# Kernel tuning notes

Hardware: AMD Instinct MI355X
Metric: run time of the kernel (lower is better)

The kernel has to match this reference:

```python
import jax, jax.numpy as jnp
import numpy as np

# ---- grid / frustum config (from default grid_config & data_config) ----
DB = (1.0, 60.0, 1.0)                 # dbound
OGH, OGW, DS = 256, 704, 16           # input size, downsample
FH, FW = OGH // DS, OGW // DS         # 16, 44
DEPTH = int(round((DB[1] - DB[0]) / DB[2]))  # 59 depth bins
NX0, NX1, NZ = 128, 128, 1            # BEV grid
DX = np.array([0.8, 0.8, 20.0], np.float32)
BX = np.array([-51.2 + 0.4, -51.2 + 0.4, 0.0], np.float32)  # row0 + dx/2


def _frustum():
    # (D, FH, FW, 3): pixel (u, v, depth)
    ds = jnp.broadcast_to(jnp.arange(DB[0], DB[1], DB[2], dtype=jnp.float32).reshape(-1, 1, 1), (DEPTH, FH, FW))
    xs = jnp.broadcast_to(jnp.linspace(0.0, OGW - 1.0, FW, dtype=jnp.float32).reshape(1, 1, FW), (DEPTH, FH, FW))
    ys = jnp.broadcast_to(jnp.linspace(0.0, OGH - 1.0, FH, dtype=jnp.float32).reshape(1, FH, 1), (DEPTH, FH, FW))
    return jnp.stack([xs, ys, ds], axis=-1)


def _geometry(rots, trans, intrins, post_rots, post_trans, bda):
    # pixel frustum -> ego-frame 3D points; (B, N, D, FH, FW, 3)
    pts = _frustum() - post_trans[:, :, None, None, None, :]
    pts = jnp.einsum('bnij,bndhwj->bndhwi', jnp.linalg.inv(post_rots), pts)
    pts = jnp.concatenate([pts[..., :2] * pts[..., 2:3], pts[..., 2:3]], axis=-1)
    comb = jnp.einsum('bnij,bnjk->bnik', rots, jnp.linalg.inv(intrins))
    pts = jnp.einsum('bnij,bndhwj->bndhwi', comb, pts) + trans[:, :, None, None, None, :]
    pts = jnp.einsum('bij,bndhwj->bndhwi', bda, pts)
    return pts


def _voxel_pool(geom, vol):
    # geom: (B,N,D,FH,FW,3), vol: (B,N,D,FH,FW,C) -> BEV (B, C*NZ, NX0, NX1)
    B, C = vol.shape[0], vol.shape[-1]
    gidx = jnp.floor((geom - (BX - DX / 2.0)) / DX).astype(jnp.int32)
    kept = ((gidx[..., 0] >= 0) & (gidx[..., 0] < NX0)
            & (gidx[..., 1] >= 0) & (gidx[..., 1] < NX1)
            & (gidx[..., 2] >= 0) & (gidx[..., 2] < NZ))
    bidx = jnp.broadcast_to(jnp.arange(B, dtype=jnp.int32).reshape(B, 1, 1, 1, 1), gidx.shape[:-1])
    flat = ((bidx * NZ + gidx[..., 2]) * NX0 + gidx[..., 0]) * NX1 + gidx[..., 1]
    nvox = B * NZ * NX0 * NX1
    flat = jnp.where(kept, flat, nvox).reshape(-1)      # dump bucket for culled pts
    feats = vol.reshape(-1, C)
    bev = jax.ops.segment_sum(feats, flat, num_segments=nvox + 1)[:nvox]
    bev = bev.reshape(B, NZ, NX0, NX1, C)
    bev = jnp.moveaxis(bev, -1, 2).reshape(B, NZ * C, NX0, NX1)  # z-major channel cat
    return bev


def setup_inputs() -> dict:
    key = jax.random.key(0)
    B, N, CIN, CT = 4, 6, 512, 64
    k1, k2 = jax.random.split(key, 2)
    x = jax.random.normal(k1, (B, N, CIN, FH, FW), dtype=jnp.float32)
    weight = jax.random.normal(k2, (DEPTH + CT, CIN), dtype=jnp.float32) * 0.02
    bias = jnp.zeros((DEPTH + CT,), dtype=jnp.float32)
    # cam->ego rotation (cam z forward -> ego x, cam x right -> ego -y, cam y down -> ego -z)
    Rcam = jnp.asarray(np.array([[0., 0., 1.], [-1., 0., 0.], [0., -1., 0.]], np.float32))
    rots = jnp.tile(Rcam, (B, N, 1, 1))
    trans = jnp.zeros((B, N, 3), dtype=jnp.float32)
    K = jnp.asarray(np.array([[600., 0., 352.], [0., 600., 128.], [0., 0., 1.]], np.float32))
    intrins = jnp.tile(K, (B, N, 1, 1))
    post_rots = jnp.tile(jnp.eye(3, dtype=jnp.float32), (B, N, 1, 1))
    post_trans = jnp.zeros((B, N, 3), dtype=jnp.float32)
    bda = jnp.tile(jnp.eye(3, dtype=jnp.float32), (B, 1, 1))
    return dict(x=x, rots=rots, trans=trans, intrins=intrins, post_rots=post_rots,
                post_trans=post_trans, bda=bda, weight=weight, bias=bias)


def reference(x, rots, trans, intrins, post_rots, post_trans, bda, weight, bias):
    # 1x1 depth/context head (eval mode): (B,N,Cin,H,W) -> (B,N,D+C,H,W)
    out = jnp.einsum('bnchw,oc->bnohw', x, weight) + bias[None, None, :, None, None]
    depth = jax.nn.softmax(out[:, :, :DEPTH], axis=2)      # (B,N,D,H,W)
    feat = out[:, :, DEPTH:]                               # (B,N,C,H,W)
    # depth-context outer product -> frustum volume (B,N,D,H,W,C)
    vol = jnp.einsum('bndhw,bnchw->bndhwc', depth, feat)
    geom = _geometry(rots, trans, intrins, post_rots, post_trans, bda)
    bev = _voxel_pool(geom, vol)                           # (B, C*NZ, 128, 128)
    return bev, depth
```

## Files before the change

kernel.cpp:

```cpp
#include <hip/hip_runtime.h>
#include <math.h>

#define CIN   512
#define NOUT  123
#define DEPN  59
#define CT    64
#define B_    4
#define N_    6
#define FH    16
#define FW    44
#define HW    704
#define NPIX  (B_*N_*HW)
#define NX    128
#define BEV_ELEMS (B_*CT*NX*NX)
#define DEPTH_OFF BEV_ELEMS

#define WS_WB   1920
#define WS_PS   (WS_WB + 32768)
#define WS_FS   (WS_PS + NPIX*64)
#define WS_GC   (WS_FS + NPIX*64)
#define WS_C    (WS_GC + NPIX*18)
#define WS_VOX  (WS_C + B_*FW*DEPN*64)

typedef short bf16x8 __attribute__((ext_vector_type(8)));
typedef float f32x4  __attribute__((ext_vector_type(4)));

__device__ inline unsigned short f2bf(float f) {
    unsigned u = __float_as_uint(f);
    return (unsigned short)((u + 0x7fffu + ((u >> 16) & 1u)) >> 16);
}

__device__ inline void inv3d(const double* m, double* o) {
    #pragma clang fp contract(off)
    double c00 = m[4]*m[8] - m[5]*m[7];
    double c01 = m[5]*m[6] - m[3]*m[8];
    double c02 = m[3]*m[7] - m[4]*m[6];
    double det = m[0]*c00 + m[1]*c01 + m[2]*c02;
    o[0] = c00/det; o[1] = (m[2]*m[7]-m[1]*m[8])/det; o[2] = (m[1]*m[5]-m[2]*m[4])/det;
    o[3] = c01/det; o[4] = (m[0]*m[8]-m[2]*m[6])/det; o[5] = (m[2]*m[3]-m[0]*m[5])/det;
    o[6] = c02/det; o[7] = (m[1]*m[6]-m[0]*m[7])/det; o[8] = (m[0]*m[4]-m[1]*m[3])/det;
}
__device__ inline void mm3d(const double* a, const double* b, double* o) {
    #pragma clang fp contract(off)
    for (int i = 0; i < 3; ++i)
        for (int k = 0; k < 3; ++k)
            o[i*3+k] = (a[i*3+0]*b[0*3+k] + a[i*3+1]*b[1*3+k]) + a[i*3+2]*b[2*3+k];
}

__global__ __launch_bounds__(256) void k0_prep(
        const float* __restrict__ rots,  const float* __restrict__ trans,
        const float* __restrict__ intr,  const float* __restrict__ prots,
        const float* __restrict__ ptrans,const float* __restrict__ bda,
        const float* __restrict__ W,     float* __restrict__ ws,
        float* __restrict__ dout) {
    __shared__ double sTd[24][33];
    const int tid = threadIdx.x;
    const int bid = blockIdx.x;
    int gtid = bid * 256 + tid;
    int stride = gridDim.x * 256;
    float4 z = {0.f, 0.f, 0.f, 0.f};
    for (int i = gtid; i < BEV_ELEMS / 4; i += stride)
        *(float4*)(dout + 4 * (size_t)i) = z;
    unsigned short* wb = (unsigned short*)(ws + WS_WB);
    for (int i = gtid; i < 128 * CIN; i += stride) {
        int o = i >> 9, c = i & 511;
        wb[i] = (o < NOUT) ? f2bf(W[o * CIN + c]) : (unsigned short)0;
    }
    if (bid >= 66) return;
    if (tid < B_ * N_) {
        #pragma clang fp contract(off)
        int t = tid, b = t / N_;
        double* X = sTd[t];
        double PR[9], Kd[9], Rd[9], Bd[9];
        for (int i = 0; i < 9; ++i) PR[i] = (double)prots[t * 9 + i];
        for (int i = 0; i < 9; ++i) Kd[i] = (double)intr[t * 9 + i];
        for (int i = 0; i < 9; ++i) Rd[i] = (double)rots[t * 9 + i];
        for (int i = 0; i < 9; ++i) Bd[i] = (double)bda[b * 9 + i];
        double iPR[9]; inv3d(PR, iPR);
        for (int i = 0; i < 9; ++i) X[i] = iPR[i];
        for (int i = 0; i < 3; ++i) X[9 + i] = (double)ptrans[t * 3 + i];
        double iK[9];  inv3d(Kd, iK);
        double comb[9]; mm3d(Rd, iK, comb);
        for (int i = 0; i < 9; ++i) X[12 + i] = comb[i];
        for (int i = 0; i < 3; ++i) X[21 + i] = (double)trans[t * 3 + i];
        for (int i = 0; i < 9; ++i) X[24 + i] = Bd[i];
    }
    __syncthreads();
    {
        #pragma clang fp contract(off)
        int i = bid * 256 + tid;
        int b = i / (FW * 96);
        int rem = i - b * (FW * 96);
        int w = rem / 96;
        int j = rem - w * 96;
        int n = j >> 4, h = j & 15;
        const double* T = sTd[b * N_ + n];
        const double xs = (w == 43) ? 703.0 : (double)w * (703.0 / 43.0);
        const double ys = (double)(h * 17);
        const double u0 = xs - T[9];
        const double u1 = ys - T[10];
        double pA[3], pB[3];
        #pragma unroll
        for (int k = 0; k < 3; ++k) {
            pA[k] = (T[3*k]*u0 + T[3*k+1]*u1) - T[3*k+2]*T[11];
            pB[k] = T[3*k+2];
        }
        double q0c[3] = { pA[0]*pA[2], pA[0]*pB[2] + pB[0]*pA[2], pB[0]*pB[2] };
        double q1c[3] = { pA[1]*pA[2], pA[1]*pB[2] + pB[1]*pA[2], pB[1]*pB[2] };
        double q2c[3] = { pA[2], pB[2], 0.0 };
        double rc[3][3], gc[3][3];
        #pragma unroll
        for (int r = 0; r < 3; ++r)
            #pragma unroll
            for (int k = 0; k < 3; ++k)
                rc[r][k] = ((T[12+3*r]*q0c[k] + T[13+3*r]*q1c[k]) + T[14+3*r]*q2c[k])
                           + ((k == 0) ? T[21+r] : 0.0);
        #pragma unroll
        for (int g = 0; g < 3; ++g)
            #pragma unroll
            for (int k = 0; k < 3; ++k)
                gc[g][k] = (T[24+3*g]*rc[0][k] + T[25+3*g]*rc[1][k]) + T[26+3*g]*rc[2][k];
        double* dst = (double*)(ws) + WS_GC / 2 + (size_t)i * 9;
        #pragma unroll
        for (int q = 0; q < 9; ++q) dst[q] = gc[q / 3][q % 3];
    }
}

#define K1A   4608
#define K1T   13824
__global__ __launch_bounds__(256, 2) void k1_gemm(const float* __restrict__ x,
                                                  const float* __restrict__ bias,
                                                  float* __restrict__ ws,
                                                  float* __restrict__ dout) {
    __shared__ __align__(16) unsigned short s16[2 * K1T];
    const int tid = threadIdx.x;
    const int wave = tid >> 6, lane = tid & 63;
    const int l15 = lane & 15, quad = lane >> 4;
    const int bn = blockIdx.y;
    const int pixbase = blockIdx.x * 64;
    const float* xg = x + (size_t)bn * CIN * HW + pixbase;
    const unsigned short* wbg = (const unsigned short*)(ws + WS_WB);
    const int cpack = tid >> 4;
    const int pix4 = (tid & 15) * 4;
    const int wo  = tid >> 3;
    const int wsub = tid & 7;

    f32x4 acc[8] = {};
    float4 xr0, xr1, xr2, xr3;
    uint4  wr4[4];
    {
        const float* src = xg + (size_t)(4 * cpack) * HW + pix4;
        xr0 = *(const float4*)(src);
        xr1 = *(const float4*)(src + HW);
        xr2 = *(const float4*)(src + 2 * HW);
        xr3 = *(const float4*)(src + 3 * HW);
        #pragma unroll
        for (int i = 0; i < 4; ++i)
            wr4[i] = *(const uint4*)(wbg + (size_t)(wo + 32 * i) * CIN + wsub * 8);
    }
    #pragma unroll
    for (int it = 0; it < 8; ++it) {
        const int buf = it & 1;
        unsigned short* sa = s16 + buf * K1T;
        unsigned short* sb = sa + K1A;
        {
            const float* f0 = (const float*)&xr0; const float* f1 = (const float*)&xr1;
            const float* f2 = (const float*)&xr2; const float* f3 = (const float*)&xr3;
            #pragma unroll
            for (int i = 0; i < 4; ++i) {
                uint2 pk;
                pk.x = (unsigned)f2bf(f0[i]) | ((unsigned)f2bf(f1[i]) << 16);
                pk.y = (unsigned)f2bf(f2[i]) | ((unsigned)f2bf(f3[i]) << 16);
                *(uint2*)&sa[(pix4 + i) * 72 + 4 * cpack] = pk;
            }
            #pragma unroll
            for (int i = 0; i < 4; ++i)
                *(uint4*)&sb[(wo + 32 * i) * 72 + wsub * 8] = wr4[i];
        }
        if (it < 7) {
            const int ck = (it + 1) * 64;
            const float* src = xg + (size_t)(ck + 4 * cpack) * HW + pix4;
            xr0 = *(const float4*)(src);
            xr1 = *(const float4*)(src + HW);
            xr2 = *(const float4*)(src + 2 * HW);
            xr3 = *(const float4*)(src + 3 * HW);
            #pragma unroll
            for (int i = 0; i < 4; ++i)
                wr4[i] = *(const uint4*)(wbg + (size_t)(wo + 32 * i) * CIN + ck + wsub * 8);
        }
        __syncthreads();
        #pragma unroll
        for (int ks = 0; ks < 64; ks += 32) {
            const bf16x8 a = *(const bf16x8*)&sa[(wave * 16 + l15) * 72 + ks + quad * 8];
            #pragma unroll
            for (int nt = 0; nt < 8; ++nt) {
                const bf16x8 b = *(const bf16x8*)&sb[(nt * 16 + l15) * 72 + ks + quad * 8];
                acc[nt] = __builtin_amdgcn_mfma_f32_16x16x32_bf16(a, b, acc[nt], 0, 0, 0);
            }
        }
    }
    float* sred = (float*)s16;
    const int b = bn / N_, n = bn - b * N_;
    {
        float bb[8];
        #pragma unroll
        for (int nt = 0; nt < 8; ++nt) {
            int o = nt * 16 + l15;
            bb[nt] = (o < NOUT) ? bias[o] : 0.0f;
        }
        float* ps = ws + WS_PS;
        float* fs = ws + WS_FS;
        #pragma unroll
        for (int reg = 0; reg < 4; ++reg) {
            int pixl = wave * 16 + quad * 4 + reg;
            int pix = pixbase + pixl;
            int h = pix / FW, w = pix - h * FW;
            size_t row = (size_t)(b * FW + w) * 96 + n * FH + h;
            float v[4]; float m = -INFINITY;
            #pragma unroll
            for (int nt = 0; nt < 4; ++nt) {
                v[nt] = acc[nt][reg] + bb[nt];
                if (nt * 16 + l15 < DEPN) m = fmaxf(m, v[nt]);
            }
            #pragma unroll
            for (int msk = 8; msk >= 1; msk >>= 1) m = fmaxf(m, __shfl_xor(m, msk, 64));
            float e[4], s = 0.0f;
            #pragma unroll
            for (int nt = 0; nt < 4; ++nt) {
                e[nt] = (nt * 16 + l15 < DEPN) ? expf(v[nt] - m) : 0.0f;
                s += e[nt];
            }
            #pragma unroll
            for (int msk = 8; msk >= 1; msk >>= 1) s += __shfl_xor(s, msk, 64);
            const float inv = 1.0f / s;
            #pragma unroll
            for (int nt = 0; nt < 4; ++nt) {
                int o = nt * 16 + l15;
                if (o < DEPN) {
                    float p = e[nt] * inv;
                    ps[row * 64 + o] = p;
                    sred[pixl * 65 + o] = p;
                } else fs[row * 64 + (o - DEPN)] = v[nt];
            }
            #pragma unroll
            for (int nt = 4; nt < 8; ++nt) {
                int o = nt * 16 + l15;
                if (o < NOUT) fs[row * 64 + (o - DEPN)] = acc[nt][reg] + bb[nt];
            }
        }
    }
    __syncthreads();
    for (int o = wave; o < DEPN; o += 4)
        dout[DEPTH_OFF + ((size_t)bn * DEPN + o) * HW + pixbase + lane] = sred[lane * 65 + o];
}

#define DQ2 16
__global__ __launch_bounds__(256) void k2b_geom(float* __restrict__ ws,
                                                float* __restrict__ dout) {
    __shared__ float sF[96][64];
    __shared__ float sP[DQ2][100];
    __shared__ unsigned short sv16[DQ2 * 96];
    __shared__ __align__(16) double sG[96 * 9];
    __shared__ int sflag[DQ2];
    const int tid = threadIdx.x;
    const int bw = blockIdx.x;
    const int b = bw / FW;
    const int dbase = blockIdx.y * DQ2;
    const int nd = min(DQ2, DEPN - dbase);

    {
        const float* fsrc = ws + WS_FS + (size_t)bw * (96 * 64);
        const float* psrc = ws + WS_PS + (size_t)bw * (96 * 64);
        for (int i = tid; i < 96 * 16; i += 256) {
            int j = i >> 4, c4 = (i & 15) * 4;
            *(float4*)&sF[j][c4] = *(const float4*)(fsrc + j * 64 + c4);
        }
        for (int i = tid; i < 96 * 4; i += 256) {
            int j = i >> 2, q = i & 3;
            const float4 p4 = *(const float4*)(psrc + j * 64 + dbase + 4 * q);
            sP[4 * q + 0][j] = p4.x; sP[4 * q + 1][j] = p4.y;
            sP[4 * q + 2][j] = p4.z; sP[4 * q + 3][j] = p4.w;
        }
        const double2* gsrc = (const double2*)((const double*)(ws) + WS_GC / 2
                                               + (size_t)bw * (96 * 9));
        for (int i = tid; i < 432; i += 256)
            ((double2*)sG)[i] = gsrc[i];
    }
    __syncthreads();

    {
        const double BXY = (double)(-51.2000007629394531f);
        for (int idx = tid; idx < nd * 96; idx += 256) {
            int dl = idx / 96, j = idx - dl * 96;
            const double* G = &sG[j * 9];
            const double dsv = (double)(dbase + dl + 1);
            const double g0 = (G[2] * dsv + G[1]) * dsv + G[0];
            const double g1 = (G[5] * dsv + G[4]) * dsv + G[3];
            const double g2 = (G[8] * dsv + G[7]) * dsv + G[6];
            const double fx = floor((g0 - BXY) * 1.25);
            const double fy = floor((g1 - BXY) * 1.25);
            const bool keep = (fx >= 0.0) & (fx < 128.0) & (fy >= 0.0) & (fy < 128.0) &
                              (g2 >= -10.0) & (g2 < 10.0);
            sv16[idx] = keep ? (unsigned short)((int)fx * NX + (int)fy)
                             : (unsigned short)0xFFFF;
        }
    }
    __syncthreads();

    {
        const int dl = tid >> 4, s = tid & 15;
        int u = -1, mix = 0;
        const int base = dl * 96 + s * 6;
        #pragma unroll
        for (int t = 0; t < 6; ++t) {
            int v = sv16[base + t];
            if (v != 0xFFFF) { if (u < 0) u = v; else if (v != u) mix = 1; }
        }
        #pragma unroll
        for (int msk = 1; msk < 16; msk <<= 1) {
            int uo = __shfl_xor(u, msk, 64);
            int mo = __shfl_xor(mix, msk, 64);
            mix = mix | mo | ((u >= 0 && uo >= 0 && uo != u) ? 1 : 0);
            u = (u < 0) ? uo : u;
        }
        if (s == 0 && dl < nd) sflag[dl] = mix ? -2 : u;
    }
    for (int idx = tid; idx < nd * 96; idx += 256) {
        if (sv16[idx] == 0xFFFF) {
            int dl = idx / 96, j = idx - dl * 96;
            sP[dl][j] = 0.0f;
        }
    }
    __syncthreads();

    const int dl = tid >> 4, ci = tid & 15;
    if (dl < nd) {
        const int flag = sflag[dl];
        if (ci == 0)
            ((int*)(ws + WS_VOX))[bw * DEPN + dbase + dl] = (flag >= 0) ? flag : -1;
        if (flag >= 0) {
            float ax = 0.f, ay = 0.f, az = 0.f, aw = 0.f;
            for (int jj = 0; jj < 96; jj += 4) {
                const float4 pv = *(const float4*)&sP[dl][jj];
                const float4 f0 = *(const float4*)&sF[jj + 0][4 * ci];
                const float4 f1 = *(const float4*)&sF[jj + 1][4 * ci];
                const float4 f2 = *(const float4*)&sF[jj + 2][4 * ci];
                const float4 f3 = *(const float4*)&sF[jj + 3][4 * ci];
                ax = fmaf(pv.x, f0.x, ax); ay = fmaf(pv.x, f0.y, ay);
                az = fmaf(pv.x, f0.z, az); aw = fmaf(pv.x, f0.w, aw);
                ax = fmaf(pv.y, f1.x, ax); ay = fmaf(pv.y, f1.y, ay);
                az = fmaf(pv.y, f1.z, az); aw = fmaf(pv.y, f1.w, aw);
                ax = fmaf(pv.z, f2.x, ax); ay = fmaf(pv.z, f2.y, ay);
                az = fmaf(pv.z, f2.z, az); aw = fmaf(pv.z, f2.w, aw);
                ax = fmaf(pv.w, f3.x, ax); ay = fmaf(pv.w, f3.y, ay);
                az = fmaf(pv.w, f3.z, az); aw = fmaf(pv.w, f3.w, aw);
            }
            float4 st = { ax, ay, az, aw };
            *(float4*)&ws[WS_C + ((size_t)(bw * DEPN + dbase + dl)) * 64 + 4 * ci] = st;
        }
    }
    for (int d2 = 0; d2 < nd; ++d2) {
        if (sflag[d2] == -2) {
            int c = tid & 63, g = tid >> 6;
            for (int jj = 0; jj < 24; ++jj) {
                int j = g * 24 + jj;
                int v = sv16[d2 * 96 + j];
                if (v != 0xFFFF)
                    atomicAdd(dout + (((size_t)(b * CT + c)) << 14) + v,
                              sP[d2][j] * sF[j][c]);
            }
        }
    }
}

#define CHUNK 128
__global__ __launch_bounds__(256) void k2c_scatter(const float* __restrict__ ws,
                                                   float* __restrict__ dout) {
    __shared__ float acc[64][CHUNK + 4];
    __shared__ int   sVox[FW * DEPN];
    __shared__ short sMatch[FW * DEPN];
    __shared__ int   nMatch;
    const int tid = threadIdx.x;
    const int base = blockIdx.x * CHUNK;
    const int b = blockIdx.y;
    for (int i = tid; i < 64 * (CHUNK + 4); i += 256) (&acc[0][0])[i] = 0.0f;
    if (tid == 0) nMatch = 0;
    const int* vsrc = (const int*)(ws + WS_VOX) + b * (FW * DEPN);
    for (int i = tid; i < FW * DEPN; i += 256) sVox[i] = vsrc[i];
    __syncthreads();
    for (int i = tid; i < FW * DEPN; i += 256) {
        int v = sVox[i];
        if ((unsigned)(v - base) < CHUNK) {
            int m = atomicAdd(&nMatch, 1);
            sMatch[m] = (short)i;
        }
    }
    __syncthreads();
    const int c = tid & 63, quarter = tid >> 6;
    const int nm = nMatch;
    for (int m = quarter; m < nm; m += 4) {
        int e = sMatch[m];
        int lv = sVox[e] - base;
        float val = ws[WS_C + ((size_t)b * (FW * DEPN) + e) * 64 + c];
        atomicAdd(&acc[c][lv], val);
    }
    __syncthreads();
    const int wave = tid >> 6, lane = tid & 63;
    float* outb = dout + (((size_t)(b * CT)) << 14) + base;
    for (int r = wave; r < 64; r += 4) {
        float2* dst = (float2*)(outb + ((size_t)r << 14) + lane * 2);
        float2 v = *dst;
        v.x += acc[r][lane * 2];
        v.y += acc[r][lane * 2 + 1];
        *dst = v;
    }
}

extern "C" void kernel_launch(void* const* d_in, const int* in_sizes, int n_in,
                              void* d_out, int out_size, void* d_ws, size_t ws_size,
                              hipStream_t stream) {
    const float* x      = (const float*)d_in[0];
    const float* rots   = (const float*)d_in[1];
    const float* trans  = (const float*)d_in[2];
    const float* intr   = (const float*)d_in[3];
    const float* prots  = (const float*)d_in[4];
    const float* ptrans = (const float*)d_in[5];
    const float* bda    = (const float*)d_in[6];
    const float* W      = (const float*)d_in[7];
    const float* bias   = (const float*)d_in[8];
    float* out = (float*)d_out;
    float* ws  = (float*)d_ws;

    k0_prep<<<512, 256, 0, stream>>>(rots, trans, intr, prots, ptrans, bda, W, ws, out);
    k1_gemm<<<dim3(HW / 64, B_ * N_), 256, 0, stream>>>(x, bias, ws, out);
    k2b_geom<<<dim3(B_ * FW, 4), 256, 0, stream>>>(ws, out);
    k2c_scatter<<<dim3(NX * NX / CHUNK, B_), 256, 0, stream>>>(ws, out);
}
```

Baseline: 150.4 us.

## Eliminate prep kernel by fusing weight conversion, geometry, and BEV zeroing into consumers

Drops the separate k0_prep launch. The GEMM now reads fp32 weights and converts them to bf16 in-register, and it also zeroes the BEV output after its epilogue. Geometry is recomputed per block in k2b_geom into shared memory, so the double-precision geometry buffer no longer goes through global memory. A global 'mixed' flag lets the scatter kernel write its results directly instead of doing a read-modify-write when no direct atomics happened. The cost is redundant weight conversion and geometry work in every block, plus an ordering dependency: the zeroing in k1 must finish before k2b's atomics, which holds because the kernels run in stream order.

```diff
diff --git a/kernel.cpp b/kernel.cpp
--- a/kernel.cpp
+++ b/kernel.cpp
@@ -18,9 +18,9 @@
 #define WS_WB   1920
 #define WS_PS   (WS_WB + 32768)
 #define WS_FS   (WS_PS + NPIX*64)
-#define WS_GC   (WS_FS + NPIX*64)
-#define WS_C    (WS_GC + NPIX*18)
+#define WS_C    (WS_FS + NPIX*64)
 #define WS_VOX  (WS_C + B_*FW*DEPN*64)
+#define WS_MIXF (WS_VOX + B_*FW*DEPN)
 
 typedef short bf16x8 __attribute__((ext_vector_type(8)));
 typedef float f32x4  __attribute__((ext_vector_type(4)));
@@ -47,30 +47,197 @@
             o[i*3+k] = (a[i*3+0]*b[0*3+k] + a[i*3+1]*b[1*3+k]) + a[i*3+2]*b[2*3+k];
 }
 
-__global__ __launch_bounds__(256) void k0_prep(
+#define K1A   4608
+#define K1T   13824
+__global__ __launch_bounds__(256, 2) void k1_gemm(const float* __restrict__ x,
+                                                  const float* __restrict__ W,
+                                                  const float* __restrict__ bias,
+                                                  float* __restrict__ ws,
+                                                  float* __restrict__ dout) {
+    __shared__ __align__(16) unsigned short s16[2 * K1T];
+    const int tid = threadIdx.x;
+    const int wave = tid >> 6, lane = tid & 63;
+    const int l15 = lane & 15, quad = lane >> 4;
+    const int bn = blockIdx.y;
+    const int pixbase = blockIdx.x * 64;
+    const float* xg = x + (size_t)bn * CIN * HW + pixbase;
+    const int cpack = tid >> 4;
+    const int pix4 = (tid & 15) * 4;
+    const int wo  = tid >> 3;
+    const int wsub = tid & 7;
+
+    f32x4 acc[8] = {};
+    float4 xr0, xr1, xr2, xr3;
+    float4 wf[8];
+    const float4 zf4 = {0.f, 0.f, 0.f, 0.f};
+    {
+        const float* src = xg + (size_t)(4 * cpack) * HW + pix4;
+        xr0 = *(const float4*)(src);
+        xr1 = *(const float4*)(src + HW);
+        xr2 = *(const float4*)(src + 2 * HW);
+        xr3 = *(const float4*)(src + 3 * HW);
+        #pragma unroll
+        for (int i = 0; i < 4; ++i) {
+            const int o = wo + 32 * i;
+            if (o < NOUT) {
+                const float* wp = W + (size_t)o * CIN + wsub * 8;
+                wf[2 * i]     = *(const float4*)(wp);
+                wf[2 * i + 1] = *(const float4*)(wp + 4);
+            } else { wf[2 * i] = zf4; wf[2 * i + 1] = zf4; }
+        }
+    }
+    #pragma unroll
+    for (int it = 0; it < 8; ++it) {
+        const int buf = it & 1;
+        unsigned short* sa = s16 + buf * K1T;
+        unsigned short* sb = sa + K1A;
+        {
+            const float* f0 = (const float*)&xr0; const float* f1 = (const float*)&xr1;
+            const float* f2 = (const float*)&xr2; const float* f3 = (const float*)&xr3;
+            #pragma unroll
+            for (int i = 0; i < 4; ++i) {
+                uint2 pk;
+                pk.x = (unsigned)f2bf(f0[i]) | ((unsigned)f2bf(f1[i]) << 16);
+                pk.y = (unsigned)f2bf(f2[i]) | ((unsigned)f2bf(f3[i]) << 16);
+                *(uint2*)&sa[(pix4 + i) * 72 + 4 * cpack] = pk;
+            }
+            #pragma unroll
+            for (int i = 0; i < 4; ++i) {
+                const float* fw = (const float*)&wf[2 * i];
+                uint4 pk;
+                pk.x = (unsigned)f2bf(fw[0]) | ((unsigned)f2bf(fw[1]) << 16);
+                pk.y = (unsigned)f2bf(fw[2]) | ((unsigned)f2bf(fw[3]) << 16);
+                pk.z = (unsigned)f2bf(fw[4]) | ((unsigned)f2bf(fw[5]) << 16);
+                pk.w = (unsigned)f2bf(fw[6]) | ((unsigned)f2bf(fw[7]) << 16);
+                *(uint4*)&sb[(wo + 32 * i) * 72 + wsub * 8] = pk;
+            }
+        }
+        if (it < 7) {
+            const int ck = (it + 1) * 64;
+            const float* src = xg + (size_t)(ck + 4 * cpack) * HW + pix4;
+            xr0 = *(const float4*)(src);
+            xr1 = *(const float4*)(src + HW);
+            xr2 = *(const float4*)(src + 2 * HW);
+            xr3 = *(const float4*)(src + 3 * HW);
+            #pragma unroll
+            for (int i = 0; i < 4; ++i) {
+                const int o = wo + 32 * i;
+                if (o < NOUT) {
+                    const float* wp = W + (size_t)o * CIN + ck + wsub * 8;
+                    wf[2 * i]     = *(const float4*)(wp);
+                    wf[2 * i + 1] = *(const float4*)(wp + 4);
+                } else { wf[2 * i] = zf4; wf[2 * i + 1] = zf4; }
+            }
+        }
+        __syncthreads();
+        #pragma unroll
+        for (int ks = 0; ks < 64; ks += 32) {
+            const bf16x8 a = *(const bf16x8*)&sa[(wave * 16 + l15) * 72 + ks + quad * 8];
+            #pragma unroll
+            for (int nt = 0; nt < 8; ++nt) {
+                const bf16x8 b = *(const bf16x8*)&sb[(nt * 16 + l15) * 72 + ks + quad * 8];
+                acc[nt] = __builtin_amdgcn_mfma_f32_16x16x32_bf16(a, b, acc[nt], 0, 0, 0);
+            }
+        }
+    }
+    float* sred = (float*)s16;
+    const int b = bn / N_, n = bn - b * N_;
+    {
+        float bb[8];
+        #pragma unroll
+        for (int nt = 0; nt < 8; ++nt) {
+            int o = nt * 16 + l15;
+            bb[nt] = (o < NOUT) ? bias[o] : 0.0f;
+        }
+        float* ps = ws + WS_PS;
+        float* fs = ws + WS_FS;
+        #pragma unroll
+        for (int reg = 0; reg < 4; ++reg) {
+            int pixl = wave * 16 + quad * 4 + reg;
+            int pix = pixbase + pixl;
+            int h = pix / FW, w = pix - h * FW;
+            size_t row = (size_t)(b * FW + w) * 96 + n * FH + h;
+            float v[4]; float m = -INFINITY;
+            #pragma unroll
+            for (int nt = 0; nt < 4; ++nt) {
+                v[nt] = acc[nt][reg] + bb[nt];
+                if (nt * 16 + l15 < DEPN) m = fmaxf(m, v[nt]);
+            }
+            #pragma unroll
+            for (int msk = 8; msk >= 1; msk >>= 1) m = fmaxf(m, __shfl_xor(m, msk, 64));
+            float e[4], s = 0.0f;
+            #pragma unroll
+            for (int nt = 0; nt < 4; ++nt) {
+                e[nt] = (nt * 16 + l15 < DEPN) ? expf(v[nt] - m) : 0.0f;
+                s += e[nt];
+            }
+            #pragma unroll
+            for (int msk = 8; msk >= 1; msk >>= 1) s += __shfl_xor(s, msk, 64);
+            const float inv = 1.0f / s;
+            #pragma unroll
+            for (int nt = 0; nt < 4; ++nt) {
+                int o = nt * 16 + l15;
+                if (o < DEPN) {
+                    float p = e[nt] * inv;
+                    ps[row * 64 + o] = p;
+                    sred[pixl * 65 + o] = p;
+                } else fs[row * 64 + (o - DEPN)] = v[nt];
+            }
+            #pragma unroll
+            for (int nt = 4; nt < 8; ++nt) {
+                int o = nt * 16 + l15;
+                if (o < NOUT) fs[row * 64 + (o - DEPN)] = acc[nt][reg] + bb[nt];
+            }
+        }
+    }
+    __syncthreads();
+    for (int o = wave; o < DEPN; o += 4)
+        dout[DEPTH_OFF + ((size_t)bn * DEPN + o) * HW + pixbase + lane] = sred[lane * 65 + o];
+    {
+        const int gbid = bn * 11 + blockIdx.x;
+        float4 z = {0.f, 0.f, 0.f, 0.f};
+        for (int i = gbid * 256 + tid; i < BEV_ELEMS / 4; i += 264 * 256)
+            *(float4*)(dout + 4 * (size_t)i) = z;
+        if (gbid == 0 && tid == 0) ((int*)(ws + WS_MIXF))[0] = 0;
+    }
+}
+
+#define DQ2 16
+__global__ __launch_bounds__(256) void k2b_geom(
         const float* __restrict__ rots,  const float* __restrict__ trans,
         const float* __restrict__ intr,  const float* __restrict__ prots,
         const float* __restrict__ ptrans,const float* __restrict__ bda,
-        const float* __restrict__ W,     float* __restrict__ ws,
-        float* __restrict__ dout) {
-    __shared__ double sTd[24][33];
+        float* __restrict__ ws,          float* __restrict__ dout) {
+    __shared__ float sF[96][64];
+    __shared__ float sP[DQ2][100];
+    __shared__ unsigned short sv16[DQ2 * 96];
+    __shared__ __align__(16) double sG[96 * 9];
+    __shared__ double sTd[N_][33];
+    __shared__ int sflag[DQ2];
     const int tid = threadIdx.x;
-    const int bid = blockIdx.x;
-    int gtid = bid * 256 + tid;
-    int stride = gridDim.x * 256;
-    float4 z = {0.f, 0.f, 0.f, 0.f};
-    for (int i = gtid; i < BEV_ELEMS / 4; i += stride)
-        *(float4*)(dout + 4 * (size_t)i) = z;
-    unsigned short* wb = (unsigned short*)(ws + WS_WB);
-    for (int i = gtid; i < 128 * CIN; i += stride) {
-        int o = i >> 9, c = i & 511;
-        wb[i] = (o < NOUT) ? f2bf(W[o * CIN + c]) : (unsigned short)0;
-    }
-    if (bid >= 66) return;
-    if (tid < B_ * N_) {
+    const int bw = blockIdx.x;
+    const int b = bw / FW, w = bw - b * FW;
+    const int dbase = blockIdx.y * DQ2;
+    const int nd = min(DQ2, DEPN - dbase);
+
+    {
+        const float* fsrc = ws + WS_FS + (size_t)bw * (96 * 64);
+        const float* psrc = ws + WS_PS + (size_t)bw * (96 * 64);
+        for (int i = tid; i < 96 * 16; i += 256) {
+            int j = i >> 4, c4 = (i & 15) * 4;
+            *(float4*)&sF[j][c4] = *(const float4*)(fsrc + j * 64 + c4);
+        }
+        for (int i = tid; i < 96 * 4; i += 256) {
+            int j = i >> 2, q = i & 3;
+            const float4 p4 = *(const float4*)(psrc + j * 64 + dbase + 4 * q);
+            sP[4 * q + 0][j] = p4.x; sP[4 * q + 1][j] = p4.y;
+            sP[4 * q + 2][j] = p4.z; sP[4 * q + 3][j] = p4.w;
+        }
+    }
+    if (tid < N_) {
         #pragma clang fp contract(off)
-        int t = tid, b = t / N_;
-        double* X = sTd[t];
+        int t = b * N_ + tid;
+        double* X = sTd[tid];
         double PR[9], Kd[9], Rd[9], Bd[9];
         for (int i = 0; i < 9; ++i) PR[i] = (double)prots[t * 9 + i];
         for (int i = 0; i < 9; ++i) Kd[i] = (double)intr[t * 9 + i];
@@ -86,15 +253,10 @@
         for (int i = 0; i < 9; ++i) X[24 + i] = Bd[i];
     }
     __syncthreads();
-    {
+    if (tid < 96) {
         #pragma clang fp contract(off)
-        int i = bid * 256 + tid;
-        int b = i / (FW * 96);
-        int rem = i - b * (FW * 96);
-        int w = rem / 96;
-        int j = rem - w * 96;
-        int n = j >> 4, h = j & 15;
-        const double* T = sTd[b * N_ + n];
+        int j = tid, n = j >> 4, h = j & 15;
+        const double* T = sTd[n];
         const double xs = (w == 43) ? 703.0 : (double)w * (703.0 / 43.0);
         const double ys = (double)(h * 17);
         const double u0 = xs - T[9];
@@ -120,171 +282,8 @@
             #pragma unroll
             for (int k = 0; k < 3; ++k)
                 gc[g][k] = (T[24+3*g]*rc[0][k] + T[25+3*g]*rc[1][k]) + T[26+3*g]*rc[2][k];
-        double* dst = (double*)(ws) + WS_GC / 2 + (size_t)i * 9;
-        #pragma unroll
-        for (int q = 0; q < 9; ++q) dst[q] = gc[q / 3][q % 3];
-    }
-}
-
-#define K1A   4608
-#define K1T   13824
-__global__ __launch_bounds__(256, 2) void k1_gemm(const float* __restrict__ x,
-                                                  const float* __restrict__ bias,
-                                                  float* __restrict__ ws,
-                                                  float* __restrict__ dout) {
-    __shared__ __align__(16) unsigned short s16[2 * K1T];
-    const int tid = threadIdx.x;
-    const int wave = tid >> 6, lane = tid & 63;
-    const int l15 = lane & 15, quad = lane >> 4;
-    const int bn = blockIdx.y;
-    const int pixbase = blockIdx.x * 64;
-    const float* xg = x + (size_t)bn * CIN * HW + pixbase;
-    const unsigned short* wbg = (const unsigned short*)(ws + WS_WB);
-    const int cpack = tid >> 4;
-    const int pix4 = (tid & 15) * 4;
-    const int wo  = tid >> 3;
-    const int wsub = tid & 7;
-
-    f32x4 acc[8] = {};
-    float4 xr0, xr1, xr2, xr3;
-    uint4  wr4[4];
-    {
-        const float* src = xg + (size_t)(4 * cpack) * HW + pix4;
-        xr0 = *(const float4*)(src);
-        xr1 = *(const float4*)(src + HW);
-        xr2 = *(const float4*)(src + 2 * HW);
-        xr3 = *(const float4*)(src + 3 * HW);
-        #pragma unroll
-        for (int i = 0; i < 4; ++i)
-            wr4[i] = *(const uint4*)(wbg + (size_t)(wo + 32 * i) * CIN + wsub * 8);
-    }
-    #pragma unroll
-    for (int it = 0; it < 8; ++it) {
-        const int buf = it & 1;
-        unsigned short* sa = s16 + buf * K1T;
-        unsigned short* sb = sa + K1A;
-        {
-            const float* f0 = (const float*)&xr0; const float* f1 = (const float*)&xr1;
-            const float* f2 = (const float*)&xr2; const float* f3 = (const float*)&xr3;
-            #pragma unroll
-            for (int i = 0; i < 4; ++i) {
-                uint2 pk;
-                pk.x = (unsigned)f2bf(f0[i]) | ((unsigned)f2bf(f1[i]) << 16);
-                pk.y = (unsigned)f2bf(f2[i]) | ((unsigned)f2bf(f3[i]) << 16);
-                *(uint2*)&sa[(pix4 + i) * 72 + 4 * cpack] = pk;
-            }
-            #pragma unroll
-            for (int i = 0; i < 4; ++i)
-                *(uint4*)&sb[(wo + 32 * i) * 72 + wsub * 8] = wr4[i];
-        }
-        if (it < 7) {
-            const int ck = (it + 1) * 64;
-            const float* src = xg + (size_t)(ck + 4 * cpack) * HW + pix4;
-            xr0 = *(const float4*)(src);
-            xr1 = *(const float4*)(src + HW);
-            xr2 = *(const float4*)(src + 2 * HW);
-            xr3 = *(const float4*)(src + 3 * HW);
-            #pragma unroll
-            for (int i = 0; i < 4; ++i)
-                wr4[i] = *(const uint4*)(wbg + (size_t)(wo + 32 * i) * CIN + ck + wsub * 8);
-        }
-        __syncthreads();
-        #pragma unroll
-        for (int ks = 0; ks < 64; ks += 32) {
-            const bf16x8 a = *(const bf16x8*)&sa[(wave * 16 + l15) * 72 + ks + quad * 8];
-            #pragma unroll
-            for (int nt = 0; nt < 8; ++nt) {
-                const bf16x8 b = *(const bf16x8*)&sb[(nt * 16 + l15) * 72 + ks + quad * 8];
-                acc[nt] = __builtin_amdgcn_mfma_f32_16x16x32_bf16(a, b, acc[nt], 0, 0, 0);
-            }
-        }
-    }
-    float* sred = (float*)s16;
-    const int b = bn / N_, n = bn - b * N_;
-    {
-        float bb[8];
-        #pragma unroll
-        for (int nt = 0; nt < 8; ++nt) {
-            int o = nt * 16 + l15;
-            bb[nt] = (o < NOUT) ? bias[o] : 0.0f;
-        }
-        float* ps = ws + WS_PS;
-        float* fs = ws + WS_FS;
-        #pragma unroll
-        for (int reg = 0; reg < 4; ++reg) {
-            int pixl = wave * 16 + quad * 4 + reg;
-            int pix = pixbase + pixl;
-            int h = pix / FW, w = pix - h * FW;
-            size_t row = (size_t)(b * FW + w) * 96 + n * FH + h;
-            float v[4]; float m = -INFINITY;
-            #pragma unroll
-            for (int nt = 0; nt < 4; ++nt) {
-                v[nt] = acc[nt][reg] + bb[nt];
-                if (nt * 16 + l15 < DEPN) m = fmaxf(m, v[nt]);
-            }
-            #pragma unroll
-            for (int msk = 8; msk >= 1; msk >>= 1) m = fmaxf(m, __shfl_xor(m, msk, 64));
-            float e[4], s = 0.0f;
-            #pragma unroll
-            for (int nt = 0; nt < 4; ++nt) {
-                e[nt] = (nt * 16 + l15 < DEPN) ? expf(v[nt] - m) : 0.0f;
-                s += e[nt];
-            }
-            #pragma unroll
-            for (int msk = 8; msk >= 1; msk >>= 1) s += __shfl_xor(s, msk, 64);
-            const float inv = 1.0f / s;
-            #pragma unroll
-            for (int nt = 0; nt < 4; ++nt) {
-                int o = nt * 16 + l15;
-                if (o < DEPN) {
-                    float p = e[nt] * inv;
-                    ps[row * 64 + o] = p;
-                    sred[pixl * 65 + o] = p;
-                } else fs[row * 64 + (o - DEPN)] = v[nt];
-            }
-            #pragma unroll
-            for (int nt = 4; nt < 8; ++nt) {
-                int o = nt * 16 + l15;
-                if (o < NOUT) fs[row * 64 + (o - DEPN)] = acc[nt][reg] + bb[nt];
-            }
-        }
-    }
-    __syncthreads();
-    for (int o = wave; o < DEPN; o += 4)
-        dout[DEPTH_OFF + ((size_t)bn * DEPN + o) * HW + pixbase + lane] = sred[lane * 65 + o];
-}
-
-#define DQ2 16
-__global__ __launch_bounds__(256) void k2b_geom(float* __restrict__ ws,
-                                                float* __restrict__ dout) {
-    __shared__ float sF[96][64];
-    __shared__ float sP[DQ2][100];
-    __shared__ unsigned short sv16[DQ2 * 96];
-    __shared__ __align__(16) double sG[96 * 9];
-    __shared__ int sflag[DQ2];
-    const int tid = threadIdx.x;
-    const int bw = blockIdx.x;
-    const int b = bw / FW;
-    const int dbase = blockIdx.y * DQ2;
-    const int nd = min(DQ2, DEPN - dbase);
-
-    {
-        const float* fsrc = ws + WS_FS + (size_t)bw * (96 * 64);
-        const float* psrc = ws + WS_PS + (size_t)bw * (96 * 64);
-        for (int i = tid; i < 96 * 16; i += 256) {
-            int j = i >> 4, c4 = (i & 15) * 4;
-            *(float4*)&sF[j][c4] = *(const float4*)(fsrc + j * 64 + c4);
-        }
-        for (int i = tid; i < 96 * 4; i += 256) {
-            int j = i >> 2, q = i & 3;
-            const float4 p4 = *(const float4*)(psrc + j * 64 + dbase + 4 * q);
-            sP[4 * q + 0][j] = p4.x; sP[4 * q + 1][j] = p4.y;
-            sP[4 * q + 2][j] = p4.z; sP[4 * q + 3][j] = p4.w;
-        }
-        const double2* gsrc = (const double2*)((const double*)(ws) + WS_GC / 2
-                                               + (size_t)bw * (96 * 9));
-        for (int i = tid; i < 432; i += 256)
-            ((double2*)sG)[i] = gsrc[i];
+        #pragma unroll
+        for (int q = 0; q < 9; ++q) sG[j * 9 + q] = gc[q / 3][q % 3];
     }
     __syncthreads();
 
@@ -361,6 +360,7 @@
     }
     for (int d2 = 0; d2 < nd; ++d2) {
         if (sflag[d2] == -2) {
+            if (tid == 0) atomicOr((int*)(ws + WS_MIXF), 1);
             int c = tid & 63, g = tid >> 6;
             for (int jj = 0; jj < 24; ++jj) {
                 int j = g * 24 + jj;
@@ -405,14 +405,22 @@
         atomicAdd(&acc[c][lv], val);
     }
     __syncthreads();
+    const int mixed = ((const int*)(ws + WS_MIXF))[0];
     const int wave = tid >> 6, lane = tid & 63;
     float* outb = dout + (((size_t)(b * CT)) << 14) + base;
-    for (int r = wave; r < 64; r += 4) {
-        float2* dst = (float2*)(outb + ((size_t)r << 14) + lane * 2);
-        float2 v = *dst;
-        v.x += acc[r][lane * 2];
-        v.y += acc[r][lane * 2 + 1];
-        *dst = v;
+    if (!mixed) {
+        for (int r = wave; r < 64; r += 4) {
+            float2 v = { acc[r][lane * 2], acc[r][lane * 2 + 1] };
+            *(float2*)(outb + ((size_t)r << 14) + lane * 2) = v;
+        }
+    } else {
+        for (int r = wave; r < 64; r += 4) {
+            float2* dst = (float2*)(outb + ((size_t)r << 14) + lane * 2);
+            float2 v = *dst;
+            v.x += acc[r][lane * 2];
+            v.y += acc[r][lane * 2 + 1];
+            *dst = v;
+        }
     }
 }
 
@@ -431,8 +439,8 @@
     float* out = (float*)d_out;
     float* ws  = (float*)d_ws;
 
-    k0_prep<<<512, 256, 0, stream>>>(rots, trans, intr, prots, ptrans, bda, W, ws, out);
-    k1_gemm<<<dim3(HW / 64, B_ * N_), 256, 0, stream>>>(x, bias, ws, out);
-    k2b_geom<<<dim3(B_ * FW, 4), 256, 0, stream>>>(ws, out);
+    k1_gemm<<<dim3(HW / 64, B_ * N_), 256, 0, stream>>>(x, W, bias, ws, out);
+    k2b_geom<<<dim3(B_ * FW, 4), 256, 0, stream>>>(rots, trans, intr, prots, ptrans,
+                                                   bda, ws, out);
     k2c_scatter<<<dim3(NX * NX / CHUNK, B_), 256, 0, stream>>>(ws, out);
 }
```

Measured after the change: 137.5 us. -8.6%, faster.
